# Kernel optimization log

Measured on AMD Instinct MI355X. Metric: run time of the kernel, lower is better.

Reference implementation:

```python
import jax, jax.numpy as jnp
import numpy as np

NEG_INF = -1.0e9  # matches torch masked_fill value (unused: no mask)

def setup_inputs() -> dict:
    key = jax.random.key(0)
    kq, kk, kv = jax.random.split(key, 3)
    B, Sq, Sk, D = 8, 2048, 2048, 512
    return {
        "query": jax.random.normal(kq, (B, Sq, D), dtype=jnp.float32),
        "key": jax.random.normal(kk, (B, Sk, D), dtype=jnp.float32),
        "value": jax.random.normal(kv, (B, Sk, D), dtype=jnp.float32),
        "temperature": jnp.ones((), dtype=jnp.float32),
    }

def reference(query, key, value, temperature):
    # Squared Euclidean distance via GEMM identity: ||q||^2 + ||k||^2 - 2 q.k
    # (same math as the broadcast sum((q-k)^2, -1), but without [B,Sq,Sk,D] tensor)
    q_sq = jnp.sum(query * query, axis=-1, keepdims=True)          # [B,Sq,1]
    k_sq = jnp.sum(key * key, axis=-1)[:, None, :]                 # [B,1,Sk]
    qk = jnp.einsum("bqd,bkd->bqk", query, key)                    # [B,Sq,Sk]
    distance_squared = q_sq + k_sq - 2.0 * qk
    similarity = -distance_squared / temperature
    attention_weights = jax.nn.softmax(similarity, axis=-1)        # [B,Sq,Sk]
    attended_values = jnp.einsum("bqk,bkd->bqd", attention_weights, value)
    return attended_values, attention_weights
```

## Files before the change

### kernel.cpp

```cpp
#include <hip/hip_runtime.h>

typedef __bf16 bf16_t;
typedef __bf16 bf16x8 __attribute__((ext_vector_type(8)));
typedef __bf16 bf16x4 __attribute__((ext_vector_type(4)));
typedef __bf16 bf16x2 __attribute__((ext_vector_type(2)));
typedef float f32x4 __attribute__((ext_vector_type(4)));

#define NB 8
#define SQ 2048
#define SK 2048
#define DD 512

#define BM 128
#define BN 128
#define BK 32
#define LDK 40

__global__ __launch_bounds__(256, 2) void logits_kernel(
    const float* __restrict__ Q, const float* __restrict__ K,
    const float* __restrict__ tempP, float* __restrict__ logits) {
  __shared__ bf16_t qh[BM][LDK], ql[BM][LDK], kh[BN][LDK], kl[BN][LDK];
  __shared__ float ksred[BN][8];
  const int b = blockIdx.z;
  const int m0 = blockIdx.y * BM;
  const int n0 = blockIdx.x * BN;
  const int tid = threadIdx.x;
  const int lane = tid & 63;
  const int wave = tid >> 6;
  const int wm = (wave >> 1) * 64;
  const int wn = (wave & 1) * 64;
  const int lrow = lane & 15;
  const int quad = lane >> 4;

  const float* Qb = Q + (size_t)b * SQ * DD;
  const float* Kb = K + (size_t)b * SK * DD;

  const int srow = tid >> 3;
  const int scol = (tid & 7) * 4;

  const float* qbase = Qb + (size_t)(m0 + srow) * DD + scol;
  const float* kbase = Kb + (size_t)(n0 + srow) * DD + scol;

  f32x4 acc[4][4];
#pragma unroll
  for (int i = 0; i < 4; i++)
#pragma unroll
    for (int j = 0; j < 4; j++) acc[i][j] = (f32x4){0.f, 0.f, 0.f, 0.f};

  float kss[4] = {0.f, 0.f, 0.f, 0.f};

  float4 pq[4], pk[4];
#pragma unroll
  for (int i = 0; i < 4; i++) {
    pq[i] = *(const float4*)(qbase + (size_t)i * 32 * DD);
    pk[i] = *(const float4*)(kbase + (size_t)i * 32 * DD);
  }

  for (int k0 = 0; k0 < DD; k0 += BK) {
    __syncthreads();
#pragma unroll
    for (int i = 0; i < 4; i++) {
      const int r = srow + i * 32;
      float4 qv = pq[i], kv = pk[i];
      bf16_t q0 = (bf16_t)qv.x, q1 = (bf16_t)qv.y, q2 = (bf16_t)qv.z, q3 = (bf16_t)qv.w;
      bf16x4 qhv = {q0, q1, q2, q3};
      bf16x4 qlv = {(bf16_t)(qv.x - (float)q0), (bf16_t)(qv.y - (float)q1),
                    (bf16_t)(qv.z - (float)q2), (bf16_t)(qv.w - (float)q3)};
      bf16_t c0 = (bf16_t)kv.x, c1 = (bf16_t)kv.y, c2 = (bf16_t)kv.z, c3 = (bf16_t)kv.w;
      bf16x4 khv = {c0, c1, c2, c3};
      bf16x4 klv = {(bf16_t)(kv.x - (float)c0), (bf16_t)(kv.y - (float)c1),
                    (bf16_t)(kv.z - (float)c2), (bf16_t)(kv.w - (float)c3)};
      *(bf16x4*)&qh[r][scol] = qhv;
      *(bf16x4*)&ql[r][scol] = qlv;
      *(bf16x4*)&kh[r][scol] = khv;
      *(bf16x4*)&kl[r][scol] = klv;
      kss[i] = fmaf(kv.x, kv.x, kss[i]);
      kss[i] = fmaf(kv.y, kv.y, kss[i]);
      kss[i] = fmaf(kv.z, kv.z, kss[i]);
      kss[i] = fmaf(kv.w, kv.w, kss[i]);
    }
    __syncthreads();

    if (k0 + BK < DD) {
#pragma unroll
      for (int i = 0; i < 4; i++) {
        pq[i] = *(const float4*)(qbase + (size_t)i * 32 * DD + (k0 + BK));
        pk[i] = *(const float4*)(kbase + (size_t)i * 32 * DD + (k0 + BK));
      }
    }

    bf16x8 bh[4], bl[4];
#pragma unroll
    for (int ni = 0; ni < 4; ni++) {
      bh[ni] = *(const bf16x8*)&kh[wn + ni * 16 + lrow][quad * 8];
      bl[ni] = *(const bf16x8*)&kl[wn + ni * 16 + lrow][quad * 8];
    }
#pragma unroll
    for (int mi = 0; mi < 4; mi++) {
      bf16x8 ah = *(const bf16x8*)&qh[wm + mi * 16 + lrow][quad * 8];
      bf16x8 al = *(const bf16x8*)&ql[wm + mi * 16 + lrow][quad * 8];
#pragma unroll
      for (int ni = 0; ni < 4; ni++) {
        acc[mi][ni] = __builtin_amdgcn_mfma_f32_16x16x32_bf16(ah, bh[ni], acc[mi][ni], 0, 0, 0);
        acc[mi][ni] = __builtin_amdgcn_mfma_f32_16x16x32_bf16(ah, bl[ni], acc[mi][ni], 0, 0, 0);
        acc[mi][ni] = __builtin_amdgcn_mfma_f32_16x16x32_bf16(al, bh[ni], acc[mi][ni], 0, 0, 0);
      }
    }
  }

#pragma unroll
  for (int i = 0; i < 4; i++) ksred[srow + i * 32][tid & 7] = kss[i];
  __syncthreads();

  const float invT = 1.0f / tempP[0];
  float* Lb = logits + (size_t)b * SQ * SK;
#pragma unroll
  for (int ni = 0; ni < 4; ni++) {
    const int nl = wn + ni * 16 + lrow;
    const int n = n0 + nl;
    const float* kr = ksred[nl];
    const float ks = ((kr[0] + kr[1]) + (kr[2] + kr[3])) +
                     ((kr[4] + kr[5]) + (kr[6] + kr[7]));
#pragma unroll
    for (int mi = 0; mi < 4; mi++) {
      const int mbase = m0 + wm + mi * 16 + quad * 4;
#pragma unroll
      for (int r = 0; r < 4; r++) {
        float s = (2.0f * acc[mi][ni][r] - ks) * invT;
        Lb[(size_t)(mbase + r) * SK + n] = s;
      }
    }
  }
}

__global__ __launch_bounds__(256) void softmax_kernel(float* __restrict__ L) {
  float* p = L + (size_t)blockIdx.x * SK;
  const int tid = threadIdx.x;
  const int wave = tid >> 6, lane = tid & 63;

  float4 a = *(const float4*)(p + tid * 4);
  float4 bv = *(const float4*)(p + 1024 + tid * 4);

  float m = fmaxf(fmaxf(fmaxf(a.x, a.y), fmaxf(a.z, a.w)),
                  fmaxf(fmaxf(bv.x, bv.y), fmaxf(bv.z, bv.w)));
#pragma unroll
  for (int off = 32; off; off >>= 1) m = fmaxf(m, __shfl_xor(m, off));
  __shared__ float redm[4];
  if (lane == 0) redm[wave] = m;
  __syncthreads();
  m = fmaxf(fmaxf(redm[0], redm[1]), fmaxf(redm[2], redm[3]));

  float e[8];
  e[0] = __expf(a.x - m);  e[1] = __expf(a.y - m);
  e[2] = __expf(a.z - m);  e[3] = __expf(a.w - m);
  e[4] = __expf(bv.x - m); e[5] = __expf(bv.y - m);
  e[6] = __expf(bv.z - m); e[7] = __expf(bv.w - m);
  float s = ((e[0] + e[1]) + (e[2] + e[3])) + ((e[4] + e[5]) + (e[6] + e[7]));
#pragma unroll
  for (int off = 32; off; off >>= 1) s += __shfl_xor(s, off);
  __shared__ float reds[4];
  if (lane == 0) reds[wave] = s;
  __syncthreads();
  s = (reds[0] + reds[1]) + (reds[2] + reds[3]);

  const float inv = 1.0f / s;
  float4 oa = {e[0] * inv, e[1] * inv, e[2] * inv, e[3] * inv};
  float4 ob = {e[4] * inv, e[5] * inv, e[6] * inv, e[7] * inv};
  *(float4*)(p + tid * 4) = oa;
  *(float4*)(p + 1024 + tid * 4) = ob;
}

__global__ __launch_bounds__(256, 2) void pv_kernel(const float* __restrict__ W,
                                                    const float* __restrict__ V,
                                                    float* __restrict__ O) {
  __shared__ bf16_t wt[BM][LDK];
  __shared__ bf16_t vt[BN][LDK];
  const int b = blockIdx.z;
  const int m0 = blockIdx.y * BM;
  const int d0 = blockIdx.x * BN;
  const int tid = threadIdx.x;
  const int lane = tid & 63;
  const int wave = tid >> 6;
  const int wm = (wave >> 1) * 64;
  const int wn = (wave & 1) * 64;
  const int lrow = lane & 15;
  const int quad = lane >> 4;

  const float* Wb = W + (size_t)b * SQ * SK;
  const float* Vb = V + (size_t)b * SK * DD;

  const int srow = tid >> 3;
  const int scol = (tid & 7) * 4;
  const int p = tid & 15;
  const int c = tid >> 4;

  const float* wbase = Wb + (size_t)(m0 + srow) * SK + scol;
  const float* vbase = Vb + (size_t)(2 * p) * DD + d0 + 4 * c;

  f32x4 acc[4][4];
#pragma unroll
  for (int i = 0; i < 4; i++)
#pragma unroll
    for (int j = 0; j < 4; j++) acc[i][j] = (f32x4){0.f, 0.f, 0.f, 0.f};

  float4 pw[4];
  float4 v0a, v1a, v0b, v1b;
#pragma unroll
  for (int i = 0; i < 4; i++) pw[i] = *(const float4*)(wbase + (size_t)i * 32 * SK);
  v0a = *(const float4*)(vbase);
  v1a = *(const float4*)(vbase + DD);
  v0b = *(const float4*)(vbase + 64);
  v1b = *(const float4*)(vbase + 64 + DD);

  for (int k0 = 0; k0 < SK; k0 += BK) {
    __syncthreads();
#pragma unroll
    for (int i = 0; i < 4; i++) {
      float4 w = pw[i];
      bf16x4 w4 = {(bf16_t)w.x, (bf16_t)w.y, (bf16_t)w.z, (bf16_t)w.w};
      *(bf16x4*)&wt[srow + i * 32][scol] = w4;
    }
    {
      bf16x2 t0 = {(bf16_t)v0a.x, (bf16_t)v1a.x};
      bf16x2 t1 = {(bf16_t)v0a.y, (bf16_t)v1a.y};
      bf16x2 t2 = {(bf16_t)v0a.z, (bf16_t)v1a.z};
      bf16x2 t3 = {(bf16_t)v0a.w, (bf16_t)v1a.w};
      *(bf16x2*)&vt[4 * c + 0][2 * p] = t0;
      *(bf16x2*)&vt[4 * c + 1][2 * p] = t1;
      *(bf16x2*)&vt[4 * c + 2][2 * p] = t2;
      *(bf16x2*)&vt[4 * c + 3][2 * p] = t3;
      bf16x2 u0 = {(bf16_t)v0b.x, (bf16_t)v1b.x};
      bf16x2 u1 = {(bf16_t)v0b.y, (bf16_t)v1b.y};
      bf16x2 u2 = {(bf16_t)v0b.z, (bf16_t)v1b.z};
      bf16x2 u3 = {(bf16_t)v0b.w, (bf16_t)v1b.w};
      *(bf16x2*)&vt[4 * c + 64 + 0][2 * p] = u0;
      *(bf16x2*)&vt[4 * c + 64 + 1][2 * p] = u1;
      *(bf16x2*)&vt[4 * c + 64 + 2][2 * p] = u2;
      *(bf16x2*)&vt[4 * c + 64 + 3][2 * p] = u3;
    }
    __syncthreads();

    if (k0 + BK < SK) {
#pragma unroll
      for (int i = 0; i < 4; i++)
        pw[i] = *(const float4*)(wbase + (size_t)i * 32 * SK + (k0 + BK));
      const float* vb = vbase + (size_t)(k0 + BK) * DD;
      v0a = *(const float4*)(vb);
      v1a = *(const float4*)(vb + DD);
      v0b = *(const float4*)(vb + 64);
      v1b = *(const float4*)(vb + 64 + DD);
    }

    bf16x8 a[4], bb[4];
#pragma unroll
    for (int mi = 0; mi < 4; mi++)
      a[mi] = *(const bf16x8*)&wt[wm + mi * 16 + lrow][quad * 8];
#pragma unroll
    for (int ni = 0; ni < 4; ni++)
      bb[ni] = *(const bf16x8*)&vt[wn + ni * 16 + lrow][quad * 8];
#pragma unroll
    for (int mi = 0; mi < 4; mi++)
#pragma unroll
      for (int ni = 0; ni < 4; ni++)
        acc[mi][ni] = __builtin_amdgcn_mfma_f32_16x16x32_bf16(a[mi], bb[ni], acc[mi][ni], 0, 0, 0);
  }

  float* Ob = O + (size_t)b * SQ * DD;
#pragma unroll
  for (int ni = 0; ni < 4; ni++) {
    const int d = d0 + wn + ni * 16 + lrow;
#pragma unroll
    for (int mi = 0; mi < 4; mi++) {
      const int mbase = m0 + wm + mi * 16 + quad * 4;
#pragma unroll
      for (int r = 0; r < 4; r++) {
        Ob[(size_t)(mbase + r) * DD + d] = acc[mi][ni][r];
      }
    }
  }
}

extern "C" void kernel_launch(void* const* d_in, const int* in_sizes, int n_in,
                              void* d_out, int out_size, void* d_ws, size_t ws_size,
                              hipStream_t stream) {
  const float* Q = (const float*)d_in[0];
  const float* K = (const float*)d_in[1];
  const float* V = (const float*)d_in[2];
  const float* T = (const float*)d_in[3];

  float* outv = (float*)d_out;
  float* logits = outv + (size_t)NB * SQ * DD;

  logits_kernel<<<dim3(SK / BN, SQ / BM, NB), 256, 0, stream>>>(Q, K, T, logits);
  softmax_kernel<<<NB * SQ, 256, 0, stream>>>(logits);
  pv_kernel<<<dim3(DD / BN, SQ / BM, NB), 256, 0, stream>>>(logits, V, outv);
}
```

Before: 459.3 us.

## Fuse softmax normalization into PV kernel using per-tile row statistics

The logits kernel now computes a per-tile row max and sum-of-exponentials and writes them to workspace. A small reduction kernel merges these into a max and inverse sum per row. A new PV kernel recomputes exp/normalize on the fly, writes the final weights and performs the PV matmul over all of D per block. This removes the standalone softmax pass over the 128 MB logits (one read and one write), at the cost of extra exp work, a different PV tiling with 32 rows per block, and dependence on workspace size (it falls back to the old path otherwise).

```diff
diff --git a/kernel.cpp b/kernel.cpp
--- a/kernel.cpp
+++ b/kernel.cpp
@@ -16,9 +16,13 @@
 #define BK 32
 #define LDK 40
 
+#define NTILE (SK / BN)
+
+template <bool doStats>
 __global__ __launch_bounds__(256, 2) void logits_kernel(
     const float* __restrict__ Q, const float* __restrict__ K,
-    const float* __restrict__ tempP, float* __restrict__ logits) {
+    const float* __restrict__ tempP, float* __restrict__ logits,
+    float2* __restrict__ partials) {
   __shared__ bf16_t qh[BM][LDK], ql[BM][LDK], kh[BN][LDK], kl[BN][LDK];
   __shared__ float ksred[BN][8];
   const int b = blockIdx.z;
@@ -126,8 +130,168 @@
       const int mbase = m0 + wm + mi * 16 + quad * 4;
 #pragma unroll
       for (int r = 0; r < 4; r++) {
-        float s = (2.0f * acc[mi][ni][r] - ks) * invT;
-        Lb[(size_t)(mbase + r) * SK + n] = s;
+        float lv = (2.0f * acc[mi][ni][r] - ks) * invT;
+        acc[mi][ni][r] = lv;
+        Lb[(size_t)(mbase + r) * SK + n] = lv;
+      }
+    }
+  }
+
+  if (doStats) {
+    float rmax[16], rsum[16];
+#pragma unroll
+    for (int mi = 0; mi < 4; mi++)
+#pragma unroll
+      for (int r = 0; r < 4; r++) {
+        float mx = fmaxf(fmaxf(acc[mi][0][r], acc[mi][1][r]),
+                         fmaxf(acc[mi][2][r], acc[mi][3][r]));
+#pragma unroll
+        for (int off = 1; off < 16; off <<= 1) mx = fmaxf(mx, __shfl_xor(mx, off));
+        rmax[mi * 4 + r] = mx;
+        float sm = __expf(acc[mi][0][r] - mx) + __expf(acc[mi][1][r] - mx) +
+                   __expf(acc[mi][2][r] - mx) + __expf(acc[mi][3][r] - mx);
+#pragma unroll
+        for (int off = 1; off < 16; off <<= 1) sm += __shfl_xor(sm, off);
+        rsum[mi * 4 + r] = sm;
+      }
+    float2* stat = (float2*)qh;
+    if (lrow == 0) {
+#pragma unroll
+      for (int mi = 0; mi < 4; mi++)
+#pragma unroll
+        for (int r = 0; r < 4; r++) {
+          const int rl = wm + mi * 16 + quad * 4 + r;
+          stat[rl * 2 + (wave & 1)] = make_float2(rmax[mi * 4 + r], rsum[mi * 4 + r]);
+        }
+    }
+    __syncthreads();
+    if (tid < BM) {
+      float2 s0 = stat[tid * 2 + 0];
+      float2 s1 = stat[tid * 2 + 1];
+      float m = fmaxf(s0.x, s1.x);
+      float s = s0.y * __expf(s0.x - m) + s1.y * __expf(s1.x - m);
+      partials[((size_t)b * SQ + m0 + tid) * NTILE + blockIdx.x] = make_float2(m, s);
+    }
+  }
+}
+
+__global__ __launch_bounds__(256) void reduce_stats_kernel(
+    const float2* __restrict__ partials, float2* __restrict__ rowstat) {
+  const int row = blockIdx.x * 256 + threadIdx.x;
+  const float2* p = partials + (size_t)row * NTILE;
+  float m = p[0].x;
+#pragma unroll
+  for (int i = 1; i < NTILE; i++) m = fmaxf(m, p[i].x);
+  float s = 0.f;
+#pragma unroll
+  for (int i = 0; i < NTILE; i++) s += p[i].y * __expf(p[i].x - m);
+  rowstat[row] = make_float2(m, 1.0f / s);
+}
+
+#define PM 32
+__global__ __launch_bounds__(256, 2) void pv_fused_kernel(
+    float* __restrict__ Wgt,
+    const float* __restrict__ V, const float2* __restrict__ rowstat,
+    float* __restrict__ O) {
+  __shared__ bf16_t wt[PM][LDK];
+  __shared__ bf16_t vt[DD][LDK];
+  const int b = blockIdx.y;
+  const int m0 = blockIdx.x * PM;
+  const int tid = threadIdx.x;
+  const int lane = tid & 63;
+  const int wave = tid >> 6;
+  const int lrow = lane & 15;
+  const int quad = lane >> 4;
+
+  float* Wb = Wgt + (size_t)b * SQ * SK;
+  const float* Vb = V + (size_t)b * SK * DD;
+
+  const int srow = tid >> 3;
+  const int scol = (tid & 7) * 4;
+  const int p = tid & 15;
+  const int c = tid >> 4;
+
+  float* wbase = Wb + (size_t)(m0 + srow) * SK + scol;
+  const float* vbase = Vb + (size_t)(2 * p) * DD + 4 * c;
+
+  const float2 rs = rowstat[(size_t)b * SQ + m0 + srow];
+  const float rm = rs.x, rinv = rs.y;
+
+  f32x4 acc[2][8];
+#pragma unroll
+  for (int i = 0; i < 2; i++)
+#pragma unroll
+    for (int j = 0; j < 8; j++) acc[i][j] = (f32x4){0.f, 0.f, 0.f, 0.f};
+
+  float4 pw;
+  float4 pv0[8], pv1[8];
+  pw = *(const float4*)(wbase);
+#pragma unroll
+  for (int j = 0; j < 8; j++) {
+    pv0[j] = *(const float4*)(vbase + 64 * j);
+    pv1[j] = *(const float4*)(vbase + 64 * j + DD);
+  }
+
+  for (int k0 = 0; k0 < SK; k0 += BK) {
+    __syncthreads();
+    {
+      float w0 = __expf(pw.x - rm) * rinv;
+      float w1 = __expf(pw.y - rm) * rinv;
+      float w2 = __expf(pw.z - rm) * rinv;
+      float w3 = __expf(pw.w - rm) * rinv;
+      bf16x4 w4 = {(bf16_t)w0, (bf16_t)w1, (bf16_t)w2, (bf16_t)w3};
+      *(bf16x4*)&wt[srow][scol] = w4;
+      float4 wout = {w0, w1, w2, w3};
+      *(float4*)(wbase + k0) = wout;
+    }
+#pragma unroll
+    for (int j = 0; j < 8; j++) {
+      const int d = 4 * c + 64 * j;
+      bf16x2 t0 = {(bf16_t)pv0[j].x, (bf16_t)pv1[j].x};
+      bf16x2 t1 = {(bf16_t)pv0[j].y, (bf16_t)pv1[j].y};
+      bf16x2 t2 = {(bf16_t)pv0[j].z, (bf16_t)pv1[j].z};
+      bf16x2 t3 = {(bf16_t)pv0[j].w, (bf16_t)pv1[j].w};
+      *(bf16x2*)&vt[d + 0][2 * p] = t0;
+      *(bf16x2*)&vt[d + 1][2 * p] = t1;
+      *(bf16x2*)&vt[d + 2][2 * p] = t2;
+      *(bf16x2*)&vt[d + 3][2 * p] = t3;
+    }
+    __syncthreads();
+
+    if (k0 + BK < SK) {
+      pw = *(const float4*)(wbase + k0 + BK);
+      const float* vb = vbase + (size_t)(k0 + BK) * DD;
+#pragma unroll
+      for (int j = 0; j < 8; j++) {
+        pv0[j] = *(const float4*)(vb + 64 * j);
+        pv1[j] = *(const float4*)(vb + 64 * j + DD);
+      }
+    }
+
+    bf16x8 a[2], bb[8];
+#pragma unroll
+    for (int mi = 0; mi < 2; mi++)
+      a[mi] = *(const bf16x8*)&wt[mi * 16 + lrow][quad * 8];
+#pragma unroll
+    for (int ni = 0; ni < 8; ni++)
+      bb[ni] = *(const bf16x8*)&vt[wave * 128 + ni * 16 + lrow][quad * 8];
+#pragma unroll
+    for (int mi = 0; mi < 2; mi++)
+#pragma unroll
+      for (int ni = 0; ni < 8; ni++)
+        acc[mi][ni] = __builtin_amdgcn_mfma_f32_16x16x32_bf16(a[mi], bb[ni], acc[mi][ni], 0, 0, 0);
+  }
+
+  float* Ob = O + (size_t)b * SQ * DD;
+#pragma unroll
+  for (int ni = 0; ni < 8; ni++) {
+    const int d = wave * 128 + ni * 16 + lrow;
+#pragma unroll
+    for (int mi = 0; mi < 2; mi++) {
+      const int mbase = m0 + mi * 16 + quad * 4;
+#pragma unroll
+      for (int r = 0; r < 4; r++) {
+        Ob[(size_t)(mbase + r) * DD + d] = acc[mi][ni][r];
       }
     }
   }
@@ -291,7 +455,20 @@
   float* outv = (float*)d_out;
   float* logits = outv + (size_t)NB * SQ * DD;
 
-  logits_kernel<<<dim3(SK / BN, SQ / BM, NB), 256, 0, stream>>>(Q, K, T, logits);
-  softmax_kernel<<<NB * SQ, 256, 0, stream>>>(logits);
-  pv_kernel<<<dim3(DD / BN, SQ / BM, NB), 256, 0, stream>>>(logits, V, outv);
-}
+  const size_t rows = (size_t)NB * SQ;
+  const size_t part_bytes = rows * NTILE * sizeof(float2);
+  const size_t stat_bytes = rows * sizeof(float2);
+  const bool fused = (ws_size >= part_bytes + stat_bytes);
+
+  if (fused) {
+    float2* partials = (float2*)d_ws;
+    float2* rowstat = (float2*)((char*)d_ws + part_bytes);
+    logits_kernel<true><<<dim3(SK / BN, SQ / BM, NB), 256, 0, stream>>>(Q, K, T, logits, partials);
+    reduce_stats_kernel<<<rows / 256, 256, 0, stream>>>(partials, rowstat);
+    pv_fused_kernel<<<dim3(SQ / PM, NB), 256, 0, stream>>>(logits, V, rowstat, outv);
+  } else {
+    logits_kernel<false><<<dim3(SK / BN, SQ / BM, NB), 256, 0, stream>>>(Q, K, T, logits, nullptr);
+    softmax_kernel<<<NB * SQ, 256, 0, stream>>>(logits);
+    pv_kernel<<<dim3(DD / BN, SQ / BM, NB), 256, 0, stream>>>(logits, V, outv);
+  }
+}
```

New measurement: 635.8 us. 38.4% more time.
